# Optimization experiments

Hardware: AMD Instinct MI355X
Metric: run time of the kernel (lower is better)

Reference implementation:

```python
import jax, jax.numpy as jnp
import numpy as np

B = 2048      # batch
L = 128       # signal_length
PL = 8        # patch_length (nodes per graph)
PS = 4        # patch_stride
LW = 4        # local_window
P = (L - PL) // PS + 1   # num_patches = 31
H = 128       # gnn/rnn hidden dim
C = 8         # num_classes


def _mean_adj():
    # A[i, j] = 1/deg(i) for 0 < |i-j| <= LW; exact mean aggregation of SAGEConv
    A = np.zeros((PL, PL), np.float32)
    for i in range(PL):
        nb = [j for j in range(PL) if 0 < abs(i - j) <= LW]
        for j in nb:
            A[i, j] = 1.0 / len(nb)
    return jnp.asarray(A)


def setup_inputs() -> dict:
    key = jax.random.key(0)
    ks = jax.random.split(key, 10)
    def n(k, shape, s):
        return jax.random.normal(k, shape, dtype=jnp.float32) * s
    inp = {
        "iq_signal": jax.random.normal(ks[0], (B, 2, L), dtype=jnp.float32),
        # SAGE layer 0 (in=2 -> H): lin_l (neighbor, with bias), lin_r (root, no bias)
        "Wl0": n(ks[1], (H, 2), 0.3), "bl0": jnp.zeros((H,), jnp.float32), "Wr0": n(ks[2], (H, 2), 0.3),
        # SAGE layers 1-2 (H -> H), stacked
        "Wl12": n(ks[3], (2, H, H), 0.08), "bl12": jnp.zeros((2, H), jnp.float32), "Wr12": n(ks[4], (2, H, H), 0.08),
        # LayerNorm params for the 3 GNN layers
        "ln_gamma": jnp.ones((3, H), jnp.float32), "ln_beta": jnp.zeros((3, H), jnp.float32),
        # 2-layer GRU (input=H, hidden=H), PyTorch gate order [r, z, n]
        "gru_w_ih": n(ks[5], (2, 3 * H, H), 0.08), "gru_w_hh": n(ks[6], (2, 3 * H, H), 0.08),
        "gru_b_ih": jnp.zeros((2, 3 * H), jnp.float32), "gru_b_hh": jnp.zeros((2, 3 * H), jnp.float32),
    }
    # ETF matrix: sqrt(C/(C-1)) * Q @ (I - J/C), Q from QR of random [H, C]
    Pm = jax.random.normal(ks[7], (H, C), dtype=jnp.float32)
    Q, _ = jnp.linalg.qr(Pm)
    I = jnp.eye(C, dtype=jnp.float32)
    J = jnp.ones((C, C), jnp.float32)
    inp["etf"] = (np.float32(np.sqrt(C / (C - 1))) * (Q @ (I - J / C))).astype(jnp.float32)
    return inp


def _layernorm(h, g, b):
    mu = h.mean(-1, keepdims=True)
    var = h.var(-1, keepdims=True)
    return (h - mu) / jnp.sqrt(var + 1e-5) * g + b


def _gru_layer(seq, w_ih, w_hh, b_ih, b_hh):
    # seq: [B, T, H]; precompute input gates for all timesteps
    xg = jnp.einsum('bti,gi->btg', seq, w_ih) + b_ih  # [B, T, 3H]
    def step(hprev, xg_t):
        hg = hprev @ w_hh.T + b_hh
        r = jax.nn.sigmoid(xg_t[:, :H] + hg[:, :H])
        z = jax.nn.sigmoid(xg_t[:, H:2 * H] + hg[:, H:2 * H])
        nn_ = jnp.tanh(xg_t[:, 2 * H:] + r * hg[:, 2 * H:])
        hnew = (1.0 - z) * nn_ + z * hprev
        return hnew, hnew
    h0 = jnp.zeros((seq.shape[0], H), seq.dtype)
    _, outs = jax.lax.scan(step, h0, xg.transpose(1, 0, 2))
    return outs.transpose(1, 0, 2)  # [B, T, H]


def reference(iq_signal, Wl0, bl0, Wr0, Wl12, bl12, Wr12, ln_gamma, ln_beta,
              gru_w_ih, gru_w_hh, gru_b_ih, gru_b_hh, etf):
    # --- DTSG: patch extraction -> [B*P, PL, 2] node features ---
    starts = jnp.arange(P) * PS
    idx = starts[:, None] + jnp.arange(PL)[None, :]       # [P, PL]
    x = iq_signal[:, :, idx]                              # [B, 2, P, PL]
    x = x.transpose(0, 2, 3, 1).reshape(B * P, PL, 2)     # [G, 8, 2]

    A = _mean_adj()  # identical graph for every patch; dense mean-aggregation

    def sage(h, Wl, bl, Wr):
        agg = jnp.einsum('ij,gjf->gif', A, h)             # mean neighbor aggregation
        return jnp.einsum('gif,of->gio', agg, Wl) + bl + jnp.einsum('gif,of->gio', h, Wr)

    # PatchGNN (dropout = identity in eval); edge_attr is ignored by PyG SAGEConv
    h = jax.nn.relu(_layernorm(sage(x, Wl0, bl0, Wr0), ln_gamma[0], ln_beta[0]))
    for i in range(2):
        hn = jax.nn.relu(_layernorm(sage(h, Wl12[i], bl12[i], Wr12[i]), ln_gamma[i + 1], ln_beta[i + 1]))
        h = h + hn  # residual (shapes match for layers 1,2)

    patch_features = h.mean(axis=1)                       # global_mean_pool -> [B*P, H]

    # --- TemporalRNN: 2-layer GRU, take last timestep ---
    seq = patch_features.reshape(B, P, H)
    o = _gru_layer(seq, gru_w_ih[0], gru_w_hh[0], gru_b_ih[0], gru_b_hh[0])
    o = _gru_layer(o, gru_w_ih[1], gru_w_hh[1], gru_b_ih[1], gru_b_hh[1])
    g = o[:, -1, :]                                       # [B, H]

    logits_g = g @ etf                                    # [B, C]
    return logits_g, g, patch_features
```

## Files before the change

### kernel.cpp

```cpp
#include <hip/hip_runtime.h>
#include <hip/hip_bf16.h>

typedef __attribute__((ext_vector_type(8))) short bf16x8;
typedef __attribute__((ext_vector_type(4))) float f32x4;

__device__ __forceinline__ unsigned short f2bf(float v) {
    union { __hip_bfloat16 h; unsigned short u; } cv;
    cv.h = __float2bfloat16(v);
    return cv.u;
}
__device__ __forceinline__ float bf2f(unsigned short u) {
    return __uint_as_float(((unsigned int)u) << 16);
}
__device__ __forceinline__ float sigm(float x) { return 1.f / (1.f + __expf(-x)); }
__device__ __forceinline__ float tanh_(float x) { return 2.f / (1.f + __expf(-2.f * x)) - 1.f; }
__device__ __forceinline__ float adjW(int i, int j) {
    const float inv[8] = {1.f/4.f, 1.f/5.f, 1.f/6.f, 1.f/7.f,
                          1.f/7.f, 1.f/6.f, 1.f/5.f, 1.f/4.f};
    int d = i - j; d = d < 0 ? -d : d;
    return (d >= 1 && d <= 4) ? inv[i] : 0.f;
}

template<int CTRL>
__device__ __forceinline__ float dppadd(float v) {
    int d = __builtin_amdgcn_update_dpp(0, __float_as_int(v), CTRL, 0xF, 0xF, true);
    return v + __int_as_float(d);
}
__device__ __forceinline__ float rowsum16(float v) {
    v = dppadd<0xB1>(v);
    v = dppadd<0x4E>(v);
    v = dppadd<0x124>(v);
    v = dppadd<0x128>(v);
    return v;
}

__global__ __launch_bounds__(256) void k0_wconv(const float* __restrict__ Wl12,
    const float* __restrict__ Wr12, const float* __restrict__ wih,
    const float* __restrict__ whh, const float* __restrict__ Wl0,
    const float* __restrict__ Wr0, unsigned short* __restrict__ wbf)
{
    int i = blockIdx.x * 256 + threadIdx.x;
    if (i < 262144) {
        float v; int base, j;
        if (i < 32768)        { v = Wl12[i];        base = (i >> 14) * 16384;           j = i & 16383; }
        else if (i < 65536)   { int s = i - 32768;  v = Wr12[s]; base = 32768 + (s >> 14) * 16384; j = s & 16383; }
        else if (i < 163840)  { int s = i - 65536;  v = wih[s];  base = 65536 + (s / 49152) * 49152; j = s % 49152; }
        else                  { int s = i - 163840; v = whh[s];  base = 163840 + (s / 49152) * 49152; j = s % 49152; }
        int col = j >> 7, k = j & 127;
        int perm = ((col >> 4) * 4 + (k >> 5)) * 512 + ((k >> 3) & 3) * 128 + (col & 15) * 8 + (k & 7);
        wbf[base + perm] = f2bf(v);
    } else {
        int e2 = i - 262144;
        int ct  = e2 >> 9;
        int off = e2 & 511;
        int li2 = off >> 7;
        int rem = off & 127;
        int colLow = rem >> 3;
        int kLow = off & 7;
        int k = li2 * 8 + kLow;
        int col = ct * 16 + colLow;
        float v = 0.f;
        if (k < 2)      v = Wl0[col * 2 + k];
        else if (k < 4) v = Wr0[col * 2 + k - 2];
        wbf[i] = f2bf(v);
    }
}

__global__ __launch_bounds__(256, 4) void k1_sage(
    const float* __restrict__ iq,
    const float* __restrict__ bl0,
    const unsigned short* __restrict__ wbf,
    const float* __restrict__ bl12,
    const float* __restrict__ lng, const float* __restrict__ lnb,
    float* __restrict__ pf)
{
    __shared__ unsigned short hT[64 * 128];
    __shared__ float statS[64][4];
    __shared__ float xS[64][2], axS[64][2];

    const int t  = threadIdx.x;
    const int l  = t & 63;
    const int w  = t >> 6;
    const int wr = w >> 1, wc = w & 1;
    const int lc = l & 15, li = l >> 4;
    const int kgrp = li * 8;
    const int half = li & 1;
    const int g0 = blockIdx.x * 8;

    if (t < 128) {
        int r = t >> 1, c = t & 1;
        int gid = g0 + (r >> 3);
        int node = r & 7;
        int b = gid / 31, p = gid - b * 31;
        xS[r][c] = iq[((size_t)b * 2 + c) * 128 + p * 4 + node];
    }
    __syncthreads();
    if (t < 128) {
        int r = t >> 1, c = t & 1;
        int node = r & 7, base = r & ~7;
        float s = 0.f;
        #pragma unroll
        for (int j = 0; j < 8; ++j) s += adjW(node, j) * xS[base + j][c];
        axS[r][c] = s;
    }
    __syncthreads();

    f32x4 acc[2][4];

    auto ln_epi = [&](const float* gptr, const float* btptr, bool resid) {
        float rs[2][4], rq[2][4];
        #pragma unroll
        for (int mt = 0; mt < 2; ++mt) {
            f32x4 sv = (acc[mt][0] + acc[mt][1]) + (acc[mt][2] + acc[mt][3]);
            f32x4 qv = acc[mt][0] * acc[mt][0] + acc[mt][1] * acc[mt][1]
                     + acc[mt][2] * acc[mt][2] + acc[mt][3] * acc[mt][3];
            #pragma unroll
            for (int q = 0; q < 4; ++q) {
                rs[mt][q] = rowsum16(sv[q]);
                rq[mt][q] = rowsum16(qv[q]);
            }
        }
        if (lc == 0) {
            #pragma unroll
            for (int mt = 0; mt < 2; ++mt)
                #pragma unroll
                for (int q = 0; q < 4; ++q) {
                    int row = wr * 32 + mt * 16 + li * 4 + q;
                    statS[row][wc * 2]     = rs[mt][q];
                    statS[row][wc * 2 + 1] = rq[mt][q];
                }
        }
        __syncthreads();
        float gam[4], bet[4];
        #pragma unroll
        for (int nt = 0; nt < 4; ++nt) {
            int col = wc * 64 + nt * 16 + lc;
            gam[nt] = gptr[col]; bet[nt] = btptr[col];
        }
        #pragma unroll
        for (int mt = 0; mt < 2; ++mt)
            #pragma unroll
            for (int q = 0; q < 4; ++q) {
                int row = wr * 32 + mt * 16 + li * 4 + q;
                int s8 = (row & 7) << 3;
                float4 st = *(const float4*)&statS[row][0];
                float sum = st.x + st.z, sq = st.y + st.w;
                float mu   = sum * (1.f / 128.f);
                float var  = sq * (1.f / 128.f) - mu * mu;
                float rstd = rsqrtf(var + 1e-5f);
                #pragma unroll
                for (int nt = 0; nt < 4; ++nt) {
                    int col = wc * 64 + nt * 16 + lc;
                    int idx = row * 128 + (col ^ s8);
                    float ag = rstd * gam[nt];
                    float bg = __builtin_fmaf(-mu, ag, bet[nt]);
                    float v  = fmaxf(__builtin_fmaf(acc[mt][nt][q], ag, bg), 0.f);
                    float hn = resid ? (bf2f(hT[idx]) + v) : v;
                    hT[idx] = f2bf(hn);
                }
            }
        __syncthreads();
    };

    {
        bf16x8 xA[2];
        #pragma unroll
        for (int mt = 0; mt < 2; ++mt) {
            bf16x8 v = (bf16x8){0, 0, 0, 0, 0, 0, 0, 0};
            if (li == 0) {
                int row = wr * 32 + mt * 16 + lc;
                v[0] = (short)f2bf(axS[row][0]); v[1] = (short)f2bf(axS[row][1]);
                v[2] = (short)f2bf(xS[row][0]);  v[3] = (short)f2bf(xS[row][1]);
            }
            xA[mt] = v;
        }
        const unsigned short* w0f = wbf + 262144;
        #pragma unroll
        for (int nt = 0; nt < 4; ++nt) {
            float bv = bl0[wc * 64 + nt * 16 + lc];
            acc[0][nt] = (f32x4){bv, bv, bv, bv};
            acc[1][nt] = (f32x4){bv, bv, bv, bv};
        }
        #pragma unroll
        for (int nt = 0; nt < 4; ++nt) {
            bf16x8 b0 = *(const bf16x8*)&w0f[(wc * 4 + nt) * 512 + l * 8];
            acc[0][nt] = __builtin_amdgcn_mfma_f32_16x16x32_bf16(xA[0], b0, acc[0][nt], 0, 0, 0);
            acc[1][nt] = __builtin_amdgcn_mfma_f32_16x16x32_bf16(xA[1], b0, acc[1][nt], 0, 0, 0);
        }
        ln_epi(lng, lnb, false);
    }

    const int aswz = (lc & 7) << 3;
    #pragma unroll 1
    for (int lay = 0; lay < 2; ++lay) {
        bf16x8 hA[2][4];
        #pragma unroll
        for (int mt = 0; mt < 2; ++mt)
            #pragma unroll
            for (int ks = 0; ks < 4; ++ks) {
                int row = wr * 32 + 16 * mt + lc;
                hA[mt][ks] = *(const bf16x8*)&hT[row * 128 + ((ks * 32 + kgrp) ^ aswz)];
            }

        const unsigned short* wl  = wbf + lay * 16384;
        const unsigned short* wrp = wbf + 32768 + lay * 16384;

        #pragma unroll
        for (int nt = 0; nt < 4; ++nt) {
            float bv = bl12[lay * 128 + wc * 64 + nt * 16 + lc];
            acc[0][nt] = (f32x4){bv, bv, bv, bv};
            acc[1][nt] = (f32x4){bv, bv, bv, bv};
        }

        #pragma unroll
        for (int ks = 0; ks < 4; ++ks) {
            #pragma unroll
            for (int nt = 0; nt < 4; ++nt) {
                bf16x8 b = *(const bf16x8*)&wl[((wc * 4 + nt) * 4 + ks) * 512 + l * 8];
                acc[0][nt] = __builtin_amdgcn_mfma_f32_16x16x32_bf16(hA[0][ks], b, acc[0][nt], 0, 0, 0);
                acc[1][nt] = __builtin_amdgcn_mfma_f32_16x16x32_bf16(hA[1][ks], b, acc[1][nt], 0, 0, 0);
            }
        }

        #pragma unroll
        for (int mt = 0; mt < 2; ++mt)
            #pragma unroll
            for (int nt = 0; nt < 4; ++nt) {
                float own[4], oth[4];
                #pragma unroll
                for (int q = 0; q < 4; ++q) {
                    own[q] = acc[mt][nt][q];
                    oth[q] = __shfl_xor(own[q], 16, 64);
                }
                float yL[4], yH[4];
                #pragma unroll
                for (int q = 0; q < 4; ++q) {
                    yL[q] = half ? oth[q] : own[q];
                    yH[q] = half ? own[q] : oth[q];
                }
                float S = yL[0]+yL[1]+yL[2]+yL[3]+yH[0]+yH[1]+yH[2]+yH[3];
                float o0, o1, o2, o3;
                if (!half) {
                    o0 = (S - yL[0] - yH[1] - yH[2] - yH[3]) * 0.25f;
                    o1 = (S - yL[1] - yH[2] - yH[3]) * 0.2f;
                    o2 = (S - yL[2] - yH[3]) * (1.f/6.f);
                    o3 = (S - yL[3]) * (1.f/7.f);
                } else {
                    o0 = (S - yH[0]) * (1.f/7.f);
                    o1 = (S - yH[1] - yL[0]) * (1.f/6.f);
                    o2 = (S - yH[2] - yL[0] - yL[1]) * 0.2f;
                    o3 = (S - yH[3] - yL[0] - yL[1] - yL[2]) * 0.25f;
                }
                acc[mt][nt][0] = o0; acc[mt][nt][1] = o1;
                acc[mt][nt][2] = o2; acc[mt][nt][3] = o3;
            }

        #pragma unroll
        for (int ks = 0; ks < 4; ++ks) {
            #pragma unroll
            for (int nt = 0; nt < 4; ++nt) {
                bf16x8 b = *(const bf16x8*)&wrp[((wc * 4 + nt) * 4 + ks) * 512 + l * 8];
                acc[0][nt] = __builtin_amdgcn_mfma_f32_16x16x32_bf16(hA[0][ks], b, acc[0][nt], 0, 0, 0);
                acc[1][nt] = __builtin_amdgcn_mfma_f32_16x16x32_bf16(hA[1][ks], b, acc[1][nt], 0, 0, 0);
            }
        }

        ln_epi(lng + (lay + 1) * 128, lnb + (lay + 1) * 128, true);
    }

    {
        const int gi = t >> 5, c0 = t & 31;
        #pragma unroll
        for (int k = 0; k < 4; ++k) {
            int c = c0 + 32 * k;
            float s = 0.f;
            #pragma unroll
            for (int j = 0; j < 8; ++j)
                s += bf2f(hT[(gi * 8 + j) * 128 + (c ^ (j << 3))]);
            pf[(size_t)(g0 + gi) * 128 + c] = s * 0.125f;
        }
    }
}

__global__ __launch_bounds__(256) void k2_xg(
    const float* __restrict__ src, const unsigned short* __restrict__ wB,
    const float* __restrict__ bias, unsigned short* __restrict__ out)
{
    const int t = threadIdx.x, w = t >> 6, l = t & 63;
    const int lc = l & 15, li = l >> 4;
    const int m0 = blockIdx.x * 64 + w * 16;

    bf16x8 aA[4];
    #pragma unroll
    for (int ks = 0; ks < 4; ++ks) {
        const float* p = src + (size_t)(m0 + lc) * 128 + ks * 32 + li * 8;
        float4 f0 = *(const float4*)p;
        float4 f1 = *(const float4*)(p + 4);
        bf16x8 v;
        v[0] = (short)f2bf(f0.x); v[1] = (short)f2bf(f0.y);
        v[2] = (short)f2bf(f0.z); v[3] = (short)f2bf(f0.w);
        v[4] = (short)f2bf(f1.x); v[5] = (short)f2bf(f1.y);
        v[6] = (short)f2bf(f1.z); v[7] = (short)f2bf(f1.w);
        aA[ks] = v;
    }
    #pragma unroll 2
    for (int ct = 0; ct < 24; ++ct) {
        float bv = bias[ct * 16 + lc];
        f32x4 acc = (f32x4){bv, bv, bv, bv};
        #pragma unroll
        for (int ks = 0; ks < 4; ++ks) {
            bf16x8 b = *(const bf16x8*)&wB[(size_t)(ct * 4 + ks) * 512 + l * 8];
            acc = __builtin_amdgcn_mfma_f32_16x16x32_bf16(aA[ks], b, acc, 0, 0, 0);
        }
        #pragma unroll
        for (int q = 0; q < 4; ++q) {
            int m = m0 + li * 4 + q;
            out[((size_t)ct * 63488 + m) * 16 + lc] = f2bf(acc[q]);
        }
    }
}

__global__ __launch_bounds__(512, 2) void k3_gru(
    const unsigned short* __restrict__ xg, const unsigned short* __restrict__ wbf,
    const float* __restrict__ bih, const float* __restrict__ bhh,
    const float* __restrict__ etf,
    float* __restrict__ gbuf, float* __restrict__ logits)
{
    __shared__ unsigned short h1S[2][16][136];
    __shared__ unsigned short h2S[2][16][136];

    const int t = threadIdx.x, w = t >> 6, l = t & 63;
    const int lc = l & 15, li = l >> 4;
    const int col = w * 16 + lc;
    const int kgrp = li * 8;
    const int b0 = blockIdx.x * 8;
    const bool act = (li < 2);

    for (int i = t; i < 2 * 16 * 136; i += 512) {
        ((unsigned short*)h1S)[i] = 0;
        ((unsigned short*)h2S)[i] = 0;
    }

    const unsigned short* wih2 = wbf + 114688;
    const unsigned short* whh1 = wbf + 163840;
    const unsigned short* whh2 = wbf + 212992;
    bf16x8 Wh1[3][4], Wi2[3][4], Wh2[3][4];
    #pragma unroll
    for (int g = 0; g < 3; ++g)
        #pragma unroll
        for (int ks = 0; ks < 4; ++ks) {
            size_t off = (size_t)((g * 8 + w) * 4 + ks) * 512 + l * 8;
            Wh1[g][ks] = *(const bf16x8*)(whh1 + off);
            Wi2[g][ks] = *(const bf16x8*)(wih2 + off);
            Wh2[g][ks] = *(const bf16x8*)(whh2 + off);
        }
    float bh1[3], bi2[3], bh2[3];
    #pragma unroll
    for (int g = 0; g < 3; ++g) {
        bh1[g] = bhh[g * 128 + col];
        bi2[g] = bih[384 + g * 128 + col];
        bh2[g] = bhh[384 + g * 128 + col];
    }

    float h1r[4] = {0.f, 0.f, 0.f, 0.f};
    float h2r[4] = {0.f, 0.f, 0.f, 0.f};
    float x1[3][4];

    auto xgld = [&](int g, int q, int ts) -> float {
        size_t m = (size_t)(b0 + li * 4 + q) * 31 + ts;
        return bf2f(xg[((size_t)(g * 8 + w) * 63488 + m) * 16 + lc]);
    };

    if (act) {
        #pragma unroll
        for (int g = 0; g < 3; ++g)
            #pragma unroll
            for (int q = 0; q < 4; ++q)
                x1[g][q] = xgld(g, q, 0);
    }
    __syncthreads();

    int cur = 0;
    for (int ts = 0; ts < 31; ++ts) {
        const int nxt = cur ^ 1;
        bf16x8 aH[4];
        #pragma unroll
        for (int ks = 0; ks < 4; ++ks) aH[ks] = *(const bf16x8*)&h1S[cur][lc][ks * 32 + kgrp];
        f32x4 acc[3];
        #pragma unroll
        for (int g = 0; g < 3; ++g) {
            acc[g] = (f32x4){0.f, 0.f, 0.f, 0.f};
            #pragma unroll
            for (int ks = 0; ks < 4; ++ks)
                acc[g] = __builtin_amdgcn_mfma_f32_16x16x32_bf16(aH[ks], Wh1[g][ks], acc[g], 0, 0, 0);
        }
        float xn[3][4];
        if (act && ts < 30) {
            #pragma unroll
            for (int g = 0; g < 3; ++g)
                #pragma unroll
                for (int q = 0; q < 4; ++q)
                    xn[g][q] = xgld(g, q, ts + 1);
        }
        if (act) {
            #pragma unroll
            for (int q = 0; q < 4; ++q) {
                float r  = sigm(x1[0][q] + acc[0][q] + bh1[0]);
                float z  = sigm(x1[1][q] + acc[1][q] + bh1[1]);
                float nn = tanh_(x1[2][q] + r * (acc[2][q] + bh1[2]));
                h1r[q] = (1.f - z) * nn + z * h1r[q];
            }
            #pragma unroll
            for (int q = 0; q < 4; ++q) h1S[nxt][li * 4 + q][col] = f2bf(h1r[q]);
        }
        __syncthreads();

        bf16x8 aH1n[4], aH2[4];
        #pragma unroll
        for (int ks = 0; ks < 4; ++ks) {
            aH1n[ks] = *(const bf16x8*)&h1S[nxt][lc][ks * 32 + kgrp];
            aH2[ks]  = *(const bf16x8*)&h2S[cur][lc][ks * 32 + kgrp];
        }
        f32x4 ax2[3], ah2[3];
        #pragma unroll
        for (int g = 0; g < 3; ++g) {
            ax2[g] = (f32x4){0.f, 0.f, 0.f, 0.f};
            ah2[g] = (f32x4){0.f, 0.f, 0.f, 0.f};
            #pragma unroll
            for (int ks = 0; ks < 4; ++ks) {
                ax2[g] = __builtin_amdgcn_mfma_f32_16x16x32_bf16(aH1n[ks], Wi2[g][ks], ax2[g], 0, 0, 0);
                ah2[g] = __builtin_amdgcn_mfma_f32_16x16x32_bf16(aH2[ks],  Wh2[g][ks], ah2[g], 0, 0, 0);
            }
        }
        if (act) {
            #pragma unroll
            for (int q = 0; q < 4; ++q) {
                float xr  = ax2[0][q] + bi2[0];
                float xz  = ax2[1][q] + bi2[1];
                float xn2 = ax2[2][q] + bi2[2];
                float r  = sigm(xr + ah2[0][q] + bh2[0]);
                float z  = sigm(xz + ah2[1][q] + bh2[1]);
                float nn = tanh_(xn2 + r * (ah2[2][q] + bh2[2]));
                h2r[q] = (1.f - z) * nn + z * h2r[q];
            }
            #pragma unroll
            for (int q = 0; q < 4; ++q) h2S[nxt][li * 4 + q][col] = f2bf(h2r[q]);
        }
        __syncthreads();

        #pragma unroll
        for (int g = 0; g < 3; ++g)
            #pragma unroll
            for (int q = 0; q < 4; ++q) x1[g][q] = xn[g][q];
        cur = nxt;
    }

    if (act) {
        #pragma unroll
        for (int q = 0; q < 4; ++q)
            gbuf[(size_t)(b0 + li * 4 + q) * 128 + col] = h2r[q];
    }

    float* fS = (float*)&h1S[0][0][0];
    __syncthreads();
    if (act) {
        #pragma unroll
        for (int q = 0; q < 4; ++q) fS[(li * 4 + q) * 128 + col] = h2r[q];
    }
    __syncthreads();
    if (t < 64) {
        int row = t >> 3, c = t & 7;
        float s = 0.f;
        #pragma unroll 8
        for (int f = 0; f < 128; ++f) s += fS[row * 128 + f] * etf[f * 8 + c];
        logits[(size_t)(b0 + row) * 8 + c] = s;
    }
}

extern "C" void kernel_launch(void* const* d_in, const int* in_sizes, int n_in,
                              void* d_out, int out_size, void* d_ws, size_t ws_size,
                              hipStream_t stream) {
    const float* iq   = (const float*)d_in[0];
    const float* Wl0  = (const float*)d_in[1];
    const float* bl0  = (const float*)d_in[2];
    const float* Wr0  = (const float*)d_in[3];
    const float* Wl12 = (const float*)d_in[4];
    const float* bl12 = (const float*)d_in[5];
    const float* Wr12 = (const float*)d_in[6];
    const float* lng  = (const float*)d_in[7];
    const float* lnb  = (const float*)d_in[8];
    const float* wih  = (const float*)d_in[9];
    const float* whh  = (const float*)d_in[10];
    const float* bih  = (const float*)d_in[11];
    const float* bhh  = (const float*)d_in[12];
    const float* etf  = (const float*)d_in[13];

    float* out    = (float*)d_out;
    float* logits = out;
    float* gbuf   = out + 16384;
    float* pf     = out + 16384 + 262144;

    unsigned short* wbf = (unsigned short*)d_ws;
    unsigned short* xg  = wbf + 266240;

    k0_wconv<<<1040, 256, 0, stream>>>(Wl12, Wr12, wih, whh, Wl0, Wr0, wbf);
    k1_sage<<<7936, 256, 0, stream>>>(iq, bl0, wbf, bl12, lng, lnb, pf);
    k2_xg<<<992, 256, 0, stream>>>(pf, wbf + 65536, bih, xg);
    k3_gru<<<256, 512, 0, stream>>>(xg, wbf, bih, bhh, etf, gbuf, logits);
}
```

Measured before the change: 307.0 us.

## Give each wave full rows so LayerNorm stats stay in-wave without barriers

The SAGE kernel's work split changes from a 2x2 wave grid (32 rows x 64 cols per wave) to each wave owning 16 full rows across all 128 columns. LayerNorm row statistics can then be reduced within one wave by cross-lane adds, which drops the shared-memory stat exchange and the two block barriers per layer. The final pooling is remapped so each wave reads only the rows it wrote. In exchange, each weight fragment loaded from global memory now feeds one MFMA instead of two, doubling B-operand load traffic per wave.

```diff
diff --git a/kernel.cpp b/kernel.cpp
--- a/kernel.cpp
+++ b/kernel.cpp
@@ -75,17 +75,16 @@
     float* __restrict__ pf)
 {
     __shared__ unsigned short hT[64 * 128];
-    __shared__ float statS[64][4];
     __shared__ float xS[64][2], axS[64][2];
 
     const int t  = threadIdx.x;
     const int l  = t & 63;
     const int w  = t >> 6;
-    const int wr = w >> 1, wc = w & 1;
     const int lc = l & 15, li = l >> 4;
     const int kgrp = li * 8;
     const int half = li & 1;
     const int g0 = blockIdx.x * 8;
+    const int rbase = w * 16;
 
     if (t < 128) {
         int r = t >> 1, c = t & 1;
@@ -105,87 +104,58 @@
     }
     __syncthreads();
 
-    f32x4 acc[2][4];
+    f32x4 acc[8];
 
     auto ln_epi = [&](const float* gptr, const float* btptr, bool resid) {
-        float rs[2][4], rq[2][4];
-        #pragma unroll
-        for (int mt = 0; mt < 2; ++mt) {
-            f32x4 sv = (acc[mt][0] + acc[mt][1]) + (acc[mt][2] + acc[mt][3]);
-            f32x4 qv = acc[mt][0] * acc[mt][0] + acc[mt][1] * acc[mt][1]
-                     + acc[mt][2] * acc[mt][2] + acc[mt][3] * acc[mt][3];
-            #pragma unroll
-            for (int q = 0; q < 4; ++q) {
-                rs[mt][q] = rowsum16(sv[q]);
-                rq[mt][q] = rowsum16(qv[q]);
-            }
-        }
-        if (lc == 0) {
-            #pragma unroll
-            for (int mt = 0; mt < 2; ++mt)
-                #pragma unroll
-                for (int q = 0; q < 4; ++q) {
-                    int row = wr * 32 + mt * 16 + li * 4 + q;
-                    statS[row][wc * 2]     = rs[mt][q];
-                    statS[row][wc * 2 + 1] = rq[mt][q];
-                }
-        }
-        __syncthreads();
-        float gam[4], bet[4];
-        #pragma unroll
-        for (int nt = 0; nt < 4; ++nt) {
-            int col = wc * 64 + nt * 16 + lc;
+        f32x4 sv = ((acc[0] + acc[1]) + (acc[2] + acc[3]))
+                 + ((acc[4] + acc[5]) + (acc[6] + acc[7]));
+        f32x4 qv = (acc[0]*acc[0] + acc[1]*acc[1]) + (acc[2]*acc[2] + acc[3]*acc[3])
+                 + (acc[4]*acc[4] + acc[5]*acc[5]) + (acc[6]*acc[6] + acc[7]*acc[7]);
+        float gam[8], bet[8];
+        #pragma unroll
+        for (int nt = 0; nt < 8; ++nt) {
+            int col = nt * 16 + lc;
             gam[nt] = gptr[col]; bet[nt] = btptr[col];
         }
         #pragma unroll
-        for (int mt = 0; mt < 2; ++mt)
-            #pragma unroll
-            for (int q = 0; q < 4; ++q) {
-                int row = wr * 32 + mt * 16 + li * 4 + q;
-                int s8 = (row & 7) << 3;
-                float4 st = *(const float4*)&statS[row][0];
-                float sum = st.x + st.z, sq = st.y + st.w;
-                float mu   = sum * (1.f / 128.f);
-                float var  = sq * (1.f / 128.f) - mu * mu;
-                float rstd = rsqrtf(var + 1e-5f);
-                #pragma unroll
-                for (int nt = 0; nt < 4; ++nt) {
-                    int col = wc * 64 + nt * 16 + lc;
-                    int idx = row * 128 + (col ^ s8);
-                    float ag = rstd * gam[nt];
-                    float bg = __builtin_fmaf(-mu, ag, bet[nt]);
-                    float v  = fmaxf(__builtin_fmaf(acc[mt][nt][q], ag, bg), 0.f);
-                    float hn = resid ? (bf2f(hT[idx]) + v) : v;
-                    hT[idx] = f2bf(hn);
-                }
-            }
-        __syncthreads();
+        for (int q = 0; q < 4; ++q) {
+            float sum = rowsum16(sv[q]);
+            float sq  = rowsum16(qv[q]);
+            int row = rbase + li * 4 + q;
+            int s8 = (row & 7) << 3;
+            float mu   = sum * (1.f / 128.f);
+            float var  = sq * (1.f / 128.f) - mu * mu;
+            float rstd = rsqrtf(var + 1e-5f);
+            #pragma unroll
+            for (int nt = 0; nt < 8; ++nt) {
+                int col = nt * 16 + lc;
+                int idx = row * 128 + (col ^ s8);
+                float ag = rstd * gam[nt];
+                float bg = __builtin_fmaf(-mu, ag, bet[nt]);
+                float v  = fmaxf(__builtin_fmaf(acc[nt][q], ag, bg), 0.f);
+                float hn = resid ? (bf2f(hT[idx]) + v) : v;
+                hT[idx] = f2bf(hn);
+            }
+        }
     };
 
     {
-        bf16x8 xA[2];
-        #pragma unroll
-        for (int mt = 0; mt < 2; ++mt) {
-            bf16x8 v = (bf16x8){0, 0, 0, 0, 0, 0, 0, 0};
-            if (li == 0) {
-                int row = wr * 32 + mt * 16 + lc;
-                v[0] = (short)f2bf(axS[row][0]); v[1] = (short)f2bf(axS[row][1]);
-                v[2] = (short)f2bf(xS[row][0]);  v[3] = (short)f2bf(xS[row][1]);
-            }
-            xA[mt] = v;
+        bf16x8 xA = (bf16x8){0, 0, 0, 0, 0, 0, 0, 0};
+        if (li == 0) {
+            int row = rbase + lc;
+            xA[0] = (short)f2bf(axS[row][0]); xA[1] = (short)f2bf(axS[row][1]);
+            xA[2] = (short)f2bf(xS[row][0]);  xA[3] = (short)f2bf(xS[row][1]);
         }
         const unsigned short* w0f = wbf + 262144;
         #pragma unroll
-        for (int nt = 0; nt < 4; ++nt) {
-            float bv = bl0[wc * 64 + nt * 16 + lc];
-            acc[0][nt] = (f32x4){bv, bv, bv, bv};
-            acc[1][nt] = (f32x4){bv, bv, bv, bv};
-        }
-        #pragma unroll
-        for (int nt = 0; nt < 4; ++nt) {
-            bf16x8 b0 = *(const bf16x8*)&w0f[(wc * 4 + nt) * 512 + l * 8];
-            acc[0][nt] = __builtin_amdgcn_mfma_f32_16x16x32_bf16(xA[0], b0, acc[0][nt], 0, 0, 0);
-            acc[1][nt] = __builtin_amdgcn_mfma_f32_16x16x32_bf16(xA[1], b0, acc[1][nt], 0, 0, 0);
+        for (int nt = 0; nt < 8; ++nt) {
+            float bv = bl0[nt * 16 + lc];
+            acc[nt] = (f32x4){bv, bv, bv, bv};
+        }
+        #pragma unroll
+        for (int nt = 0; nt < 8; ++nt) {
+            bf16x8 b0 = *(const bf16x8*)&w0f[nt * 512 + l * 8];
+            acc[nt] = __builtin_amdgcn_mfma_f32_16x16x32_bf16(xA, b0, acc[nt], 0, 0, 0);
         }
         ln_epi(lng, lnb, false);
     }
@@ -193,75 +163,66 @@
     const int aswz = (lc & 7) << 3;
     #pragma unroll 1
     for (int lay = 0; lay < 2; ++lay) {
-        bf16x8 hA[2][4];
-        #pragma unroll
-        for (int mt = 0; mt < 2; ++mt)
-            #pragma unroll
-            for (int ks = 0; ks < 4; ++ks) {
-                int row = wr * 32 + 16 * mt + lc;
-                hA[mt][ks] = *(const bf16x8*)&hT[row * 128 + ((ks * 32 + kgrp) ^ aswz)];
-            }
+        bf16x8 hA[4];
+        #pragma unroll
+        for (int ks = 0; ks < 4; ++ks)
+            hA[ks] = *(const bf16x8*)&hT[(rbase + lc) * 128 + ((ks * 32 + kgrp) ^ aswz)];
 
         const unsigned short* wl  = wbf + lay * 16384;
         const unsigned short* wrp = wbf + 32768 + lay * 16384;
 
         #pragma unroll
-        for (int nt = 0; nt < 4; ++nt) {
-            float bv = bl12[lay * 128 + wc * 64 + nt * 16 + lc];
-            acc[0][nt] = (f32x4){bv, bv, bv, bv};
-            acc[1][nt] = (f32x4){bv, bv, bv, bv};
+        for (int nt = 0; nt < 8; ++nt) {
+            float bv = bl12[lay * 128 + nt * 16 + lc];
+            acc[nt] = (f32x4){bv, bv, bv, bv};
         }
 
         #pragma unroll
         for (int ks = 0; ks < 4; ++ks) {
             #pragma unroll
-            for (int nt = 0; nt < 4; ++nt) {
-                bf16x8 b = *(const bf16x8*)&wl[((wc * 4 + nt) * 4 + ks) * 512 + l * 8];
-                acc[0][nt] = __builtin_amdgcn_mfma_f32_16x16x32_bf16(hA[0][ks], b, acc[0][nt], 0, 0, 0);
-                acc[1][nt] = __builtin_amdgcn_mfma_f32_16x16x32_bf16(hA[1][ks], b, acc[1][nt], 0, 0, 0);
-            }
-        }
-
-        #pragma unroll
-        for (int mt = 0; mt < 2; ++mt)
-            #pragma unroll
-            for (int nt = 0; nt < 4; ++nt) {
-                float own[4], oth[4];
-                #pragma unroll
-                for (int q = 0; q < 4; ++q) {
-                    own[q] = acc[mt][nt][q];
-                    oth[q] = __shfl_xor(own[q], 16, 64);
-                }
-                float yL[4], yH[4];
-                #pragma unroll
-                for (int q = 0; q < 4; ++q) {
-                    yL[q] = half ? oth[q] : own[q];
-                    yH[q] = half ? own[q] : oth[q];
-                }
-                float S = yL[0]+yL[1]+yL[2]+yL[3]+yH[0]+yH[1]+yH[2]+yH[3];
-                float o0, o1, o2, o3;
-                if (!half) {
-                    o0 = (S - yL[0] - yH[1] - yH[2] - yH[3]) * 0.25f;
-                    o1 = (S - yL[1] - yH[2] - yH[3]) * 0.2f;
-                    o2 = (S - yL[2] - yH[3]) * (1.f/6.f);
-                    o3 = (S - yL[3]) * (1.f/7.f);
-                } else {
-                    o0 = (S - yH[0]) * (1.f/7.f);
-                    o1 = (S - yH[1] - yL[0]) * (1.f/6.f);
-                    o2 = (S - yH[2] - yL[0] - yL[1]) * 0.2f;
-                    o3 = (S - yH[3] - yL[0] - yL[1] - yL[2]) * 0.25f;
-                }
-                acc[mt][nt][0] = o0; acc[mt][nt][1] = o1;
-                acc[mt][nt][2] = o2; acc[mt][nt][3] = o3;
-            }
+            for (int nt = 0; nt < 8; ++nt) {
+                bf16x8 b = *(const bf16x8*)&wl[(nt * 4 + ks) * 512 + l * 8];
+                acc[nt] = __builtin_amdgcn_mfma_f32_16x16x32_bf16(hA[ks], b, acc[nt], 0, 0, 0);
+            }
+        }
+
+        #pragma unroll
+        for (int nt = 0; nt < 8; ++nt) {
+            float own[4], oth[4];
+            #pragma unroll
+            for (int q = 0; q < 4; ++q) {
+                own[q] = acc[nt][q];
+                oth[q] = __shfl_xor(own[q], 16, 64);
+            }
+            float yL[4], yH[4];
+            #pragma unroll
+            for (int q = 0; q < 4; ++q) {
+                yL[q] = half ? oth[q] : own[q];
+                yH[q] = half ? own[q] : oth[q];
+            }
+            float S = yL[0]+yL[1]+yL[2]+yL[3]+yH[0]+yH[1]+yH[2]+yH[3];
+            float o0, o1, o2, o3;
+            if (!half) {
+                o0 = (S - yL[0] - yH[1] - yH[2] - yH[3]) * 0.25f;
+                o1 = (S - yL[1] - yH[2] - yH[3]) * 0.2f;
+                o2 = (S - yL[2] - yH[3]) * (1.f/6.f);
+                o3 = (S - yL[3]) * (1.f/7.f);
+            } else {
+                o0 = (S - yH[0]) * (1.f/7.f);
+                o1 = (S - yH[1] - yL[0]) * (1.f/6.f);
+                o2 = (S - yH[2] - yL[0] - yL[1]) * 0.2f;
+                o3 = (S - yH[3] - yL[0] - yL[1] - yL[2]) * 0.25f;
+            }
+            acc[nt][0] = o0; acc[nt][1] = o1;
+            acc[nt][2] = o2; acc[nt][3] = o3;
+        }
 
         #pragma unroll
         for (int ks = 0; ks < 4; ++ks) {
             #pragma unroll
-            for (int nt = 0; nt < 4; ++nt) {
-                bf16x8 b = *(const bf16x8*)&wrp[((wc * 4 + nt) * 4 + ks) * 512 + l * 8];
-                acc[0][nt] = __builtin_amdgcn_mfma_f32_16x16x32_bf16(hA[0][ks], b, acc[0][nt], 0, 0, 0);
-                acc[1][nt] = __builtin_amdgcn_mfma_f32_16x16x32_bf16(hA[1][ks], b, acc[1][nt], 0, 0, 0);
+            for (int nt = 0; nt < 8; ++nt) {
+                bf16x8 b = *(const bf16x8*)&wrp[(nt * 4 + ks) * 512 + l * 8];
+                acc[nt] = __builtin_amdgcn_mfma_f32_16x16x32_bf16(hA[ks], b, acc[nt], 0, 0, 0);
             }
         }
 
@@ -269,7 +230,8 @@
     }
 
     {
-        const int gi = t >> 5, c0 = t & 31;
+        const int gsel = l >> 5, c0 = l & 31;
+        const int gi = 2 * w + gsel;
         #pragma unroll
         for (int k = 0; k < 4; ++k) {
             int c = c0 + 32 * k;
```

New measurement: 325.6 us. +6.1%, slower.
